# Kernel tuning notes

Hardware: AMD Instinct MI355X
Metric: run time of the kernel (lower is better)

Reference implementation:

```python
import jax, jax.numpy as jnp
import numpy as np

PZ = 16          # partition_size
ITERS = 3        # soft_skel iterations
ADP_SMOOTH = 1e-08
A = 0.5
B = 0.5
THRESHOLD = 0.8


def _blockify(x, pz):
    # x: (N, C, Z, X, Y) -> (N*nz*nx*ny, C, pz, pz, pz), loop order N,z,x,y
    N, C, Z, X, Y = x.shape
    nz, nx, ny = Z // pz, X // pz, Y // pz
    x = x.reshape(N, C, nz, pz, nx, pz, ny, pz)
    x = x.transpose(0, 2, 4, 6, 1, 3, 5, 7)
    return x.reshape(N * nz * nx * ny, C, pz, pz, pz)


def _maxpool3d(x, win, pad):
    # torch max_pool pads with -inf
    return jax.lax.reduce_window(
        x, -jnp.inf, jax.lax.max,
        (1, 1) + win, (1, 1, 1, 1, 1),
        ((0, 0), (0, 0), (pad[0], pad[0]), (pad[1], pad[1]), (pad[2], pad[2])))


def _minpool3d(x, win, pad):
    # -maxpool(-x) == minpool with +inf padding
    return jax.lax.reduce_window(
        x, jnp.inf, jax.lax.min,
        (1, 1) + win, (1, 1, 1, 1, 1),
        ((0, 0), (0, 0), (pad[0], pad[0]), (pad[1], pad[1]), (pad[2], pad[2])))


def _soft_erode(img):
    p1 = _minpool3d(img, (3, 1, 1), (1, 0, 0))
    p2 = _minpool3d(img, (1, 3, 1), (0, 1, 0))
    p3 = _minpool3d(img, (1, 1, 3), (0, 0, 1))
    return jnp.minimum(jnp.minimum(p1, p2), p3)


def _soft_dilate(img):
    return _maxpool3d(img, (3, 3, 3), (1, 1, 1))


def _soft_skel(img, iters):
    img1 = _soft_dilate(_soft_erode(img))
    skel = jax.nn.relu(img - img1)
    for _ in range(iters):
        img = _soft_erode(img)
        img1 = _soft_dilate(_soft_erode(img))
        delta = jax.nn.relu(img - img1)
        skel = skel + jax.nn.relu(delta - skel * delta)
    return skel


def _laplacian_bdr(x):
    # 3x3x3 kernel: all -1 with center 26; per-block conv, zero padding 1
    k = -jnp.ones((27,), dtype=x.dtype).at[13].set(26.0).reshape(1, 1, 3, 3, 3)
    b = jax.lax.conv_general_dilated(
        x, k, window_strides=(1, 1, 1), padding=[(1, 1)] * 3,
        dimension_numbers=('NCDHW', 'OIDHW', 'NCDHW'))
    # clamp(min=0) then threshold at 0.1 -> binary map (zero gradient, as in torch)
    return (b > 0.1).astype(x.dtype)


def _per_channel_dice(p, g, eps=1e-6):
    C = p.shape[1]
    pf = jnp.moveaxis(p, 1, 0).reshape(C, -1)
    gf = jnp.moveaxis(g, 1, 0).reshape(C, -1)
    intersect = jnp.sum(pf * gf, axis=-1)
    denom = jnp.sum(pf * pf, axis=-1) + jnp.sum(gf * gf, axis=-1)
    return 2.0 * intersect / jnp.maximum(denom, eps)


def _tversky_terms(p_blk, g_blk):
    # blocks: (M, C, pz, pz, pz) -> per-block adaptive Tversky loss sum
    M = p_blk.shape[0]
    pf = p_blk.reshape(M, -1)
    gf = g_blk.reshape(M, -1)
    tp = jnp.sum(gf * pf, axis=1)
    fn = jnp.sum(gf * (1.0 - pf), axis=1)
    fp = jnp.sum((1.0 - gf) * pf, axis=1)
    alpha = A + B * ((fp + ADP_SMOOTH) / (fp + fn + ADP_SMOOTH))
    beta = A + B * ((fn + ADP_SMOOTH) / (fp + fn + ADP_SMOOTH))
    return jnp.sum(1.0 - (tp + ADP_SMOOTH) / (tp + alpha * fp + beta * fn + ADP_SMOOTH))


def _forward(pred, groundtruth, w1, w2):
    dice_coeff = jnp.mean(_per_channel_dice(pred, groundtruth))
    dice_loss = 1.0 - jnp.mean(_per_channel_dice(pred, groundtruth))

    p_blk = _blockify(pred, PZ)          # (M, 1, pz, pz, pz)
    g_blk = _blockify(groundtruth, PZ)
    M = p_blk.shape[0]

    pre_bdr = _laplacian_bdr(p_blk)
    gt_bdr = _laplacian_bdr(g_blk)
    pre_cl = _soft_skel(p_blk, ITERS)
    gt_cl = _soft_skel(g_blk, ITERS)

    loss_bdr = _tversky_terms(pre_bdr, gt_bdr)
    loss_cl = _tversky_terms(pre_cl, gt_cl)

    w1s, w2s = w1[0], w2[0]
    edge_loss = (w1s ** -2 * loss_bdr + w2s ** -2 * loss_cl) / (2.0 * M) \
        + jnp.log(1.0 + jnp.abs(w1s) * jnp.abs(w2s))

    return jnp.where(dice_coeff < THRESHOLD, dice_loss, dice_loss + edge_loss)


def setup_inputs() -> dict:
    key = jax.random.key(0)
    k1, k2 = jax.random.split(key)
    shape = (2, 1, 192, 192, 192)
    gt = (jax.random.uniform(k1, shape, dtype=jnp.float32) > 0.7).astype(jnp.float32)
    # pred close to gt so dice_coeff > threshold and the adaptive branch runs
    pred = jnp.clip(gt * 0.9 + 0.05 + 0.02 * jax.random.normal(k2, shape, dtype=jnp.float32), 0.0, 1.0)
    return {
        'pred': pred,
        'groundtruth': gt,
        'w1': jnp.ones((1,), dtype=jnp.float32),
        'w2': jnp.ones((1,), dtype=jnp.float32),
    }


def reference(pred, groundtruth, w1, w2):
    return _forward(pred, groundtruth, w1, w2)
```

## Files before the change

kernel.cpp:

```cpp
#include <hip/hip_runtime.h>
#include <cmath>

#define NBLK 3456

template<int CTRL>
__device__ __forceinline__ int updpp(int oldv, int v) {
  return __builtin_amdgcn_update_dpp(oldv, v, CTRL, 0xF, 0xF, false);
}
__device__ __forceinline__ float nbr_lo_f(float v, float pad, bool ylo) {
  float t = __int_as_float(updpp<0x111>(__float_as_int(pad), __float_as_int(v)));
  return ylo ? pad : t;
}
__device__ __forceinline__ float nbr_hi_f(float v, float pad, bool yhi) {
  float t = __int_as_float(updpp<0x101>(__float_as_int(pad), __float_as_int(v)));
  return yhi ? pad : t;
}
__device__ __forceinline__ unsigned nbr_lo_u(unsigned v, unsigned pad, bool ylo) {
  unsigned t = (unsigned)updpp<0x111>((int)pad, (int)v);
  return ylo ? pad : t;
}
__device__ __forceinline__ unsigned nbr_hi_u(unsigned v, unsigned pad, bool yhi) {
  unsigned t = (unsigned)updpp<0x101>((int)pad, (int)v);
  return yhi ? pad : t;
}

#define COL_IDX(c, xx) (((c)*18 + (xx) + 1)*16 + y)

__global__ __launch_bounds__(256)
void fused_blocks(const float* __restrict__ pred, const float* __restrict__ gtp,
                  float* __restrict__ ws)
{
  __shared__ float4   bufE[1152];
  __shared__ float4   bufT[1152];
  __shared__ unsigned m_ex[288];
  __shared__ float    red[36];

  const int tid = threadIdx.x;
  const int x = tid >> 4;
  const int y = tid & 15;
  const bool ylo = (y == 0), yhi = (y == 15);

  const int b  = blockIdx.x;
  const int n  = b / 1728;
  const int r  = b - n * 1728;
  const int bz = r / 144;
  const int r2 = r - bz * 144;
  const int bx = r2 / 12;
  const int by = r2 - bx * 12;

  const size_t base = (size_t)(n * 192 + bz * 16) * 36864
                    + (size_t)(bx * 16 + x) * 192 + (size_t)(by * 16 + y);

  const float INF = __builtin_inff();

  if (tid < 128) {
    const int c  = tid >> 5;
    const int xi = ((tid >> 4) & 1) ? 17 : 0;
    const int yy = tid & 15;
    const int idx = (c * 18 + xi) * 16 + yy;
    bufE[idx] = make_float4(INF, INF, INF, INF);
    bufT[idx] = make_float4(0.f, 0.f, 0.f, 0.f);
  }

  float p[16];
  #pragma unroll
  for (int z = 0; z < 16; ++z) p[z] = pred[base + (size_t)z * 36864];

  float sp2 = 0.f;
  #pragma unroll
  for (int z = 0; z < 16; ++z) sp2 = fmaf(p[z], p[z], sp2);

  #pragma unroll
  for (int c = 0; c < 4; ++c)
    bufE[COL_IDX(c, x)] = make_float4(p[4*c], p[4*c+1], p[4*c+2], p[4*c+3]);

  __syncthreads();

  float szy[16];
  {
    float sy[16];
    #pragma unroll
    for (int z = 0; z < 16; ++z) {
      float v = p[z];
      sy[z] = v + nbr_lo_f(v, 0.f, ylo) + nbr_hi_f(v, 0.f, yhi);
    }
    #pragma unroll
    for (int z = 0; z < 16; ++z) {
      float s = sy[z];
      if (z > 0)  s += sy[z-1];
      if (z < 15) s += sy[z+1];
      szy[z] = s;
    }
  }
  #pragma unroll
  for (int c = 0; c < 4; ++c)
    bufT[COL_IDX(c, x)] = make_float4(szy[4*c], szy[4*c+1], szy[4*c+2], szy[4*c+3]);
  __syncthreads();

  unsigned pm_bdr = 0u;
  #pragma unroll
  for (int c = 0; c < 4; ++c) {
    float4 a4 = bufT[COL_IDX(c, x - 1)];
    float4 b4 = bufT[COL_IDX(c, x + 1)];
    float sm0 = a4.x + b4.x, sm1 = a4.y + b4.y, sm2 = a4.z + b4.z, sm3 = a4.w + b4.w;
    float bb0 = fmaf(27.f, p[4*c+0], -(szy[4*c+0] + sm0));
    float bb1 = fmaf(27.f, p[4*c+1], -(szy[4*c+1] + sm1));
    float bb2 = fmaf(27.f, p[4*c+2], -(szy[4*c+2] + sm2));
    float bb3 = fmaf(27.f, p[4*c+3], -(szy[4*c+3] + sm3));
    if (bb0 > 0.1f) pm_bdr |= (1u << (4*c+0));
    if (bb1 > 0.1f) pm_bdr |= (1u << (4*c+1));
    if (bb2 > 0.1f) pm_bdr |= (1u << (4*c+2));
    if (bb3 > 0.1f) pm_bdr |= (1u << (4*c+3));
  }
  __syncthreads();
  if (tid < 128) {
    const int c  = tid >> 5;
    const int xi = ((tid >> 4) & 1) ? 17 : 0;
    const int yy = tid & 15;
    bufT[(c * 18 + xi) * 16 + yy] = make_float4(-INF, -INF, -INF, -INF);
  }

  float cur[16], skl[16];
  #pragma unroll
  for (int z = 0; z < 16; ++z) { cur[z] = p[z]; skl[z] = 0.f; }

  for (int k = 0; k < 4; ++k) {
    float xm[16], xp[16], en[16];
    #pragma unroll
    for (int c = 0; c < 4; ++c) {
      float4 a4 = bufE[COL_IDX(c, x - 1)];
      float4 b4 = bufE[COL_IDX(c, x + 1)];
      xm[4*c] = a4.x; xm[4*c+1] = a4.y; xm[4*c+2] = a4.z; xm[4*c+3] = a4.w;
      xp[4*c] = b4.x; xp[4*c+1] = b4.y; xp[4*c+2] = b4.z; xp[4*c+3] = b4.w;
    }
    #pragma unroll
    for (int z = 0; z < 16; ++z) {
      float v = cur[z];
      float m = fminf(v, fminf(nbr_lo_f(v, INF, ylo), nbr_hi_f(v, INF, yhi)));
      if (z > 0)  m = fminf(m, cur[z-1]);
      if (z < 15) m = fminf(m, cur[z+1]);
      en[z] = fminf(m, fminf(xm[z], xp[z]));
    }
    __syncthreads();
    #pragma unroll
    for (int c = 0; c < 4; ++c)
      bufE[COL_IDX(c, x)] = make_float4(en[4*c], en[4*c+1], en[4*c+2], en[4*c+3]);
    float ty[16], tz[16];
    #pragma unroll
    for (int z = 0; z < 16; ++z) {
      float v = en[z];
      ty[z] = fmaxf(v, fmaxf(nbr_lo_f(v, -INF, ylo), nbr_hi_f(v, -INF, yhi)));
    }
    #pragma unroll
    for (int z = 0; z < 16; ++z) {
      float m = ty[z];
      if (z > 0)  m = fmaxf(m, ty[z-1]);
      if (z < 15) m = fmaxf(m, ty[z+1]);
      tz[z] = m;
    }
    __syncthreads();
    #pragma unroll
    for (int c = 0; c < 4; ++c)
      bufT[COL_IDX(c, x)] = make_float4(tz[4*c], tz[4*c+1], tz[4*c+2], tz[4*c+3]);
    __syncthreads();
    #pragma unroll
    for (int c = 0; c < 4; ++c) {
      float4 a4 = bufT[COL_IDX(c, x - 1)];
      float4 b4 = bufT[COL_IDX(c, x + 1)];
      float dm[4] = {fmaxf(a4.x, b4.x), fmaxf(a4.y, b4.y),
                     fmaxf(a4.z, b4.z), fmaxf(a4.w, b4.w)};
      #pragma unroll
      for (int j = 0; j < 4; ++j) {
        const int z = 4*c + j;
        float D = fmaxf(tz[z], dm[j]);
        float delta = fmaxf(cur[z] - D, 0.f);
        skl[z] += fmaxf(fmaf(-skl[z], delta, delta), 0.f);
        cur[z] = en[z];
      }
    }
  }

  float spg = 0.f;
  unsigned gm = 0u;
  {
    float g[16];
    #pragma unroll
    for (int z = 0; z < 16; ++z) g[z] = gtp[base + (size_t)z * 36864];
    #pragma unroll
    for (int z = 0; z < 16; ++z) {
      spg = fmaf(p[z], g[z], spg);
      if (g[z] > 0.5f) gm |= (1u << z);
    }
  }

  unsigned ly  = gm & nbr_lo_u(gm, 0u, ylo) & nbr_hi_u(gm, 0u, yhi);
  unsigned lzy = ly & (ly >> 1) & ((ly << 1) & 0xFFFFu);
  m_ex[(x + 1) * 16 + y] = lzy;
  if (tid < 32) m_ex[((tid >> 4) ? 17 : 0) * 16 + (tid & 15)] = 0u;
  __syncthreads();
  unsigned gm_bdr = gm & ~(m_ex[x * 16 + y] & lzy & m_ex[(x + 2) * 16 + y]);

  unsigned curm = gm, sklm = 0u;
  for (int k = 0; k < 4; ++k) {
    __syncthreads();
    m_ex[(x + 1) * 16 + y] = curm;
    if (tid < 32) m_ex[((tid >> 4) ? 17 : 0) * 16 + (tid & 15)] = 0xFFFFu;
    __syncthreads();
    unsigned em = curm
        & nbr_lo_u(curm, 0xFFFFu, ylo) & nbr_hi_u(curm, 0xFFFFu, yhi)
        & ((curm >> 1) | 0x8000u) & ((curm << 1) | 1u)
        & m_ex[x * 16 + y] & m_ex[(x + 2) * 16 + y];
    em &= 0xFFFFu;
    unsigned dy  = em | nbr_lo_u(em, 0u, ylo) | nbr_hi_u(em, 0u, yhi);
    unsigned dzy = (dy | (dy >> 1) | (dy << 1)) & 0xFFFFu;
    __syncthreads();
    m_ex[(x + 1) * 16 + y] = dzy;
    if (tid < 32) m_ex[((tid >> 4) ? 17 : 0) * 16 + (tid & 15)] = 0u;
    __syncthreads();
    unsigned D = m_ex[x * 16 + y] | dzy | m_ex[(x + 2) * 16 + y];
    sklm |= curm & ~D;
    curm = em;
  }

  float vals[9];
  {
    float tcl = 0.f, scl = 0.f;
    #pragma unroll
    for (int z = 0; z < 16; ++z) {
      scl += skl[z];
      tcl += ((sklm >> z) & 1u) ? skl[z] : 0.f;
    }
    vals[0] = tcl;
    vals[1] = scl;
    vals[2] = (float)__popc(sklm);
    vals[3] = (float)__popc(pm_bdr & gm_bdr);
    vals[4] = (float)__popc(pm_bdr);
    vals[5] = (float)__popc(gm_bdr);
    vals[6] = spg;
    vals[7] = sp2;
    vals[8] = (float)__popc(gm);
  }
  #pragma unroll
  for (int j = 0; j < 9; ++j) {
    float v = vals[j];
    #pragma unroll
    for (int off = 32; off; off >>= 1) v += __shfl_xor(v, off);
    vals[j] = v;
  }
  if ((tid & 63) == 0) {
    #pragma unroll
    for (int j = 0; j < 9; ++j) red[(tid >> 6) * 9 + j] = vals[j];
  }
  __syncthreads();
  if (tid == 0) {
    float t[9];
    #pragma unroll
    for (int j = 0; j < 9; ++j) t[j] = red[j] + red[9 + j] + red[18 + j] + red[27 + j];
    const float s = 1e-8f;
    float tp = t[3], fp = t[4] - t[3], fn = t[5] - t[3];
    float den = fp + fn + s;
    float alpha = 0.5f + 0.5f * ((fp + s) / den);
    float beta  = 0.5f + 0.5f * ((fn + s) / den);
    float lb = 1.f - (tp + s) / (tp + alpha * fp + beta * fn + s);
    float tpc = t[0], fpc = t[1] - t[0], fnc = t[2] - t[0];
    float denc = fpc + fnc + s;
    float alphac = 0.5f + 0.5f * ((fpc + s) / denc);
    float betac  = 0.5f + 0.5f * ((fnc + s) / denc);
    float lc = 1.f - (tpc + s) / (tpc + alphac * fpc + betac * fnc + s);
    float* o = ws + (size_t)b * 8;
    o[0] = lb; o[1] = lc; o[2] = t[6]; o[3] = t[7]; o[4] = t[8];
  }
}

__global__ __launch_bounds__(256)
void finalize_kernel(const float* __restrict__ ws, const float* __restrict__ w1p,
                     const float* __restrict__ w2p, float* __restrict__ out)
{
  __shared__ double red2[20];
  double a[5] = {0.0, 0.0, 0.0, 0.0, 0.0};
  for (int i = threadIdx.x; i < NBLK; i += 256) {
    const float* o = ws + (size_t)i * 8;
    a[0] += (double)o[0];
    a[1] += (double)o[1];
    a[2] += (double)o[2];
    a[3] += (double)o[3];
    a[4] += (double)o[4];
  }
  #pragma unroll
  for (int j = 0; j < 5; ++j) {
    double v = a[j];
    #pragma unroll
    for (int off = 32; off; off >>= 1) v += __shfl_xor(v, off);
    if ((threadIdx.x & 63) == 0) red2[(threadIdx.x >> 6) * 5 + j] = v;
  }
  __syncthreads();
  if (threadIdx.x == 0) {
    double t[5];
    #pragma unroll
    for (int j = 0; j < 5; ++j) t[j] = red2[j] + red2[5 + j] + red2[10 + j] + red2[15 + j];
    double denom = t[3] + t[4];
    if (denom < 1e-6) denom = 1e-6;
    double dice = 2.0 * t[2] / denom;
    double dl = 1.0 - dice;
    double w1 = (double)w1p[0], w2 = (double)w2p[0];
    double edge = (t[0] / (w1 * w1) + t[1] / (w2 * w2)) / (2.0 * (double)NBLK)
                + log(1.0 + fabs(w1) * fabs(w2));
    out[0] = (float)((dice < 0.8) ? dl : (dl + edge));
  }
}

extern "C" void kernel_launch(void* const* d_in, const int* in_sizes, int n_in,
                              void* d_out, int out_size, void* d_ws, size_t ws_size,
                              hipStream_t stream)
{
  const float* pred = (const float*)d_in[0];
  const float* gtp  = (const float*)d_in[1];
  const float* w1   = (const float*)d_in[2];
  const float* w2   = (const float*)d_in[3];
  float* ws = (float*)d_ws;

  fused_blocks<<<NBLK, 256, 0, stream>>>(pred, gtp, ws);
  finalize_kernel<<<1, 256, 0, stream>>>(ws, w1, w2, (float*)d_out);
}
```

Measured before the change: 178.3 us.

## Merge LDS buffers, use DPP bound_ctrl padding, fuse finalize via atomics

Collapses the two float4 shared buffers and mask and reduction arrays into one aliased LDS buffer, and sets launch bounds to 8 blocks per CU to raise occupancy. Replaces the explicit y-boundary selects with DPP bound_ctrl zero-fill or keep-self semantics, which is valid for min/max since the lane itself is already in the window. Moves the ground-truth load up to overlap with the pred load. Drops the separate finalize kernel in favour of float atomics plus a last-block ticket, with a memset to zero the accumulators. Float atomic accumulation order is nondeterministic, and the lower per-thread register budget from the occupancy target may cause spills.

```diff
diff --git a/kernel.cpp b/kernel.cpp
--- a/kernel.cpp
+++ b/kernel.cpp
@@ -3,42 +3,43 @@
 
 #define NBLK 3456
 
+#define DPP_SHR1 0x111
+#define DPP_SHL1 0x101
+
 template<int CTRL>
-__device__ __forceinline__ int updpp(int oldv, int v) {
-  return __builtin_amdgcn_update_dpp(oldv, v, CTRL, 0xF, 0xF, false);
-}
-__device__ __forceinline__ float nbr_lo_f(float v, float pad, bool ylo) {
-  float t = __int_as_float(updpp<0x111>(__float_as_int(pad), __float_as_int(v)));
-  return ylo ? pad : t;
-}
-__device__ __forceinline__ float nbr_hi_f(float v, float pad, bool yhi) {
-  float t = __int_as_float(updpp<0x101>(__float_as_int(pad), __float_as_int(v)));
-  return yhi ? pad : t;
-}
-__device__ __forceinline__ unsigned nbr_lo_u(unsigned v, unsigned pad, bool ylo) {
-  unsigned t = (unsigned)updpp<0x111>((int)pad, (int)v);
-  return ylo ? pad : t;
-}
-__device__ __forceinline__ unsigned nbr_hi_u(unsigned v, unsigned pad, bool yhi) {
-  unsigned t = (unsigned)updpp<0x101>((int)pad, (int)v);
-  return yhi ? pad : t;
+__device__ __forceinline__ float dpp_keep_f(float v) {
+  return __int_as_float(__builtin_amdgcn_update_dpp(
+      __float_as_int(v), __float_as_int(v), CTRL, 0xF, 0xF, false));
+}
+template<int CTRL>
+__device__ __forceinline__ float dpp_zero_f(float v) {
+  return __int_as_float(__builtin_amdgcn_update_dpp(
+      0, __float_as_int(v), CTRL, 0xF, 0xF, true));
+}
+template<int CTRL>
+__device__ __forceinline__ unsigned dpp_keep_u(unsigned v) {
+  return (unsigned)__builtin_amdgcn_update_dpp((int)v, (int)v, CTRL, 0xF, 0xF, false);
+}
+template<int CTRL>
+__device__ __forceinline__ unsigned dpp_zero_u(unsigned v) {
+  return (unsigned)__builtin_amdgcn_update_dpp(0, (int)v, CTRL, 0xF, 0xF, true);
 }
 
 #define COL_IDX(c, xx) (((c)*18 + (xx) + 1)*16 + y)
 
-__global__ __launch_bounds__(256)
+__global__ __launch_bounds__(256, 8)
 void fused_blocks(const float* __restrict__ pred, const float* __restrict__ gtp,
-                  float* __restrict__ ws)
+                  const float* __restrict__ w1p, const float* __restrict__ w2p,
+                  float* __restrict__ acc,
+                  float* __restrict__ out)
 {
-  __shared__ float4   bufE[1152];
-  __shared__ float4   bufT[1152];
-  __shared__ unsigned m_ex[288];
-  __shared__ float    red[36];
+  __shared__ float4 buf[1152];
+  unsigned* m_ex = (unsigned*)buf;
+  float*    red  = ((float*)buf) + 512;
 
   const int tid = threadIdx.x;
   const int x = tid >> 4;
   const int y = tid & 15;
-  const bool ylo = (y == 0), yhi = (y == 15);
 
   const int b  = blockIdx.x;
   const int n  = b / 1728;
@@ -53,28 +54,28 @@
 
   const float INF = __builtin_inff();
 
-  if (tid < 128) {
-    const int c  = tid >> 5;
-    const int xi = ((tid >> 4) & 1) ? 17 : 0;
-    const int yy = tid & 15;
-    const int idx = (c * 18 + xi) * 16 + yy;
-    bufE[idx] = make_float4(INF, INF, INF, INF);
-    bufT[idx] = make_float4(0.f, 0.f, 0.f, 0.f);
-  }
+  auto write_pads = [&](float pv) {
+    if (tid < 128) {
+      const int c  = tid >> 5;
+      const int xi = ((tid >> 4) & 1) ? 17 : 0;
+      const int yy = tid & 15;
+      buf[(c * 18 + xi) * 16 + yy] = make_float4(pv, pv, pv, pv);
+    }
+  };
 
   float p[16];
   #pragma unroll
   for (int z = 0; z < 16; ++z) p[z] = pred[base + (size_t)z * 36864];
 
-  float sp2 = 0.f;
-  #pragma unroll
-  for (int z = 0; z < 16; ++z) sp2 = fmaf(p[z], p[z], sp2);
-
-  #pragma unroll
-  for (int c = 0; c < 4; ++c)
-    bufE[COL_IDX(c, x)] = make_float4(p[4*c], p[4*c+1], p[4*c+2], p[4*c+3]);
-
-  __syncthreads();
+  unsigned gm = 0u;
+  float sp2 = 0.f, spg = 0.f;
+  #pragma unroll
+  for (int z = 0; z < 16; ++z) {
+    float gz = gtp[base + (size_t)z * 36864];
+    sp2 = fmaf(p[z], p[z], sp2);
+    spg = fmaf(p[z], gz, spg);
+    if (gz > 0.5f) gm |= (1u << z);
+  }
 
   float szy[16];
   {
@@ -82,7 +83,7 @@
     #pragma unroll
     for (int z = 0; z < 16; ++z) {
       float v = p[z];
-      sy[z] = v + nbr_lo_f(v, 0.f, ylo) + nbr_hi_f(v, 0.f, yhi);
+      sy[z] = v + dpp_zero_f<DPP_SHR1>(v) + dpp_zero_f<DPP_SHL1>(v);
     }
     #pragma unroll
     for (int z = 0; z < 16; ++z) {
@@ -94,62 +95,58 @@
   }
   #pragma unroll
   for (int c = 0; c < 4; ++c)
-    bufT[COL_IDX(c, x)] = make_float4(szy[4*c], szy[4*c+1], szy[4*c+2], szy[4*c+3]);
+    buf[COL_IDX(c, x)] = make_float4(szy[4*c], szy[4*c+1], szy[4*c+2], szy[4*c+3]);
+  write_pads(0.f);
   __syncthreads();
 
   unsigned pm_bdr = 0u;
   #pragma unroll
   for (int c = 0; c < 4; ++c) {
-    float4 a4 = bufT[COL_IDX(c, x - 1)];
-    float4 b4 = bufT[COL_IDX(c, x + 1)];
-    float sm0 = a4.x + b4.x, sm1 = a4.y + b4.y, sm2 = a4.z + b4.z, sm3 = a4.w + b4.w;
-    float bb0 = fmaf(27.f, p[4*c+0], -(szy[4*c+0] + sm0));
-    float bb1 = fmaf(27.f, p[4*c+1], -(szy[4*c+1] + sm1));
-    float bb2 = fmaf(27.f, p[4*c+2], -(szy[4*c+2] + sm2));
-    float bb3 = fmaf(27.f, p[4*c+3], -(szy[4*c+3] + sm3));
-    if (bb0 > 0.1f) pm_bdr |= (1u << (4*c+0));
-    if (bb1 > 0.1f) pm_bdr |= (1u << (4*c+1));
-    if (bb2 > 0.1f) pm_bdr |= (1u << (4*c+2));
-    if (bb3 > 0.1f) pm_bdr |= (1u << (4*c+3));
-  }
-  __syncthreads();
-  if (tid < 128) {
-    const int c  = tid >> 5;
-    const int xi = ((tid >> 4) & 1) ? 17 : 0;
-    const int yy = tid & 15;
-    bufT[(c * 18 + xi) * 16 + yy] = make_float4(-INF, -INF, -INF, -INF);
-  }
+    float4 a4 = buf[COL_IDX(c, x - 1)];
+    float4 b4 = buf[COL_IDX(c, x + 1)];
+    float sm[4] = {a4.x + b4.x, a4.y + b4.y, a4.z + b4.z, a4.w + b4.w};
+    #pragma unroll
+    for (int j = 0; j < 4; ++j) {
+      const int z = 4*c + j;
+      float bb = fmaf(27.f, p[z], -(szy[z] + sm[j]));
+      if (bb > 0.1f) pm_bdr |= (1u << z);
+    }
+  }
+  __syncthreads();
+
+  #pragma unroll
+  for (int c = 0; c < 4; ++c)
+    buf[COL_IDX(c, x)] = make_float4(p[4*c], p[4*c+1], p[4*c+2], p[4*c+3]);
+  write_pads(INF);
+  __syncthreads();
 
   float cur[16], skl[16];
   #pragma unroll
   for (int z = 0; z < 16; ++z) { cur[z] = p[z]; skl[z] = 0.f; }
 
   for (int k = 0; k < 4; ++k) {
-    float xm[16], xp[16], en[16];
+    float xm[16], xp[16];
     #pragma unroll
     for (int c = 0; c < 4; ++c) {
-      float4 a4 = bufE[COL_IDX(c, x - 1)];
-      float4 b4 = bufE[COL_IDX(c, x + 1)];
+      float4 a4 = buf[COL_IDX(c, x - 1)];
+      float4 b4 = buf[COL_IDX(c, x + 1)];
       xm[4*c] = a4.x; xm[4*c+1] = a4.y; xm[4*c+2] = a4.z; xm[4*c+3] = a4.w;
       xp[4*c] = b4.x; xp[4*c+1] = b4.y; xp[4*c+2] = b4.z; xp[4*c+3] = b4.w;
     }
+    float en[16];
     #pragma unroll
     for (int z = 0; z < 16; ++z) {
       float v = cur[z];
-      float m = fminf(v, fminf(nbr_lo_f(v, INF, ylo), nbr_hi_f(v, INF, yhi)));
+      float m = fminf(v, fminf(dpp_keep_f<DPP_SHR1>(v), dpp_keep_f<DPP_SHL1>(v)));
       if (z > 0)  m = fminf(m, cur[z-1]);
       if (z < 15) m = fminf(m, cur[z+1]);
       en[z] = fminf(m, fminf(xm[z], xp[z]));
     }
-    __syncthreads();
-    #pragma unroll
-    for (int c = 0; c < 4; ++c)
-      bufE[COL_IDX(c, x)] = make_float4(en[4*c], en[4*c+1], en[4*c+2], en[4*c+3]);
     float ty[16], tz[16];
     #pragma unroll
     for (int z = 0; z < 16; ++z) {
       float v = en[z];
-      ty[z] = fmaxf(v, fmaxf(nbr_lo_f(v, -INF, ylo), nbr_hi_f(v, -INF, yhi)));
+      ty[z] = fmaxf(v, fmaxf(dpp_keep_f<DPP_SHR1>(v), dpp_keep_f<DPP_SHL1>(v)));
     }
     #pragma unroll
     for (int z = 0; z < 16; ++z) {
@@ -161,12 +158,13 @@
     __syncthreads();
     #pragma unroll
     for (int c = 0; c < 4; ++c)
-      bufT[COL_IDX(c, x)] = make_float4(tz[4*c], tz[4*c+1], tz[4*c+2], tz[4*c+3]);
+      buf[COL_IDX(c, x)] = make_float4(tz[4*c], tz[4*c+1], tz[4*c+2], tz[4*c+3]);
+    write_pads(-INF);
     __syncthreads();
     #pragma unroll
     for (int c = 0; c < 4; ++c) {
-      float4 a4 = bufT[COL_IDX(c, x - 1)];
-      float4 b4 = bufT[COL_IDX(c, x + 1)];
+      float4 a4 = buf[COL_IDX(c, x - 1)];
+      float4 b4 = buf[COL_IDX(c, x + 1)];
       float dm[4] = {fmaxf(a4.x, b4.x), fmaxf(a4.y, b4.y),
                      fmaxf(a4.z, b4.z), fmaxf(a4.w, b4.w)};
       #pragma unroll
@@ -178,22 +176,18 @@
         cur[z] = en[z];
       }
     }
-  }
-
-  float spg = 0.f;
-  unsigned gm = 0u;
-  {
-    float g[16];
-    #pragma unroll
-    for (int z = 0; z < 16; ++z) g[z] = gtp[base + (size_t)z * 36864];
-    #pragma unroll
-    for (int z = 0; z < 16; ++z) {
-      spg = fmaf(p[z], g[z], spg);
-      if (g[z] > 0.5f) gm |= (1u << z);
-    }
-  }
-
-  unsigned ly  = gm & nbr_lo_u(gm, 0u, ylo) & nbr_hi_u(gm, 0u, yhi);
+    if (k < 3) {
+      __syncthreads();
+      #pragma unroll
+      for (int c = 0; c < 4; ++c)
+        buf[COL_IDX(c, x)] = make_float4(en[4*c], en[4*c+1], en[4*c+2], en[4*c+3]);
+      write_pads(INF);
+      __syncthreads();
+    }
+  }
+  __syncthreads();
+
+  unsigned ly  = gm & dpp_zero_u<DPP_SHR1>(gm) & dpp_zero_u<DPP_SHL1>(gm);
   unsigned lzy = ly & (ly >> 1) & ((ly << 1) & 0xFFFFu);
   m_ex[(x + 1) * 16 + y] = lzy;
   if (tid < 32) m_ex[((tid >> 4) ? 17 : 0) * 16 + (tid & 15)] = 0u;
@@ -207,11 +201,11 @@
     if (tid < 32) m_ex[((tid >> 4) ? 17 : 0) * 16 + (tid & 15)] = 0xFFFFu;
     __syncthreads();
     unsigned em = curm
-        & nbr_lo_u(curm, 0xFFFFu, ylo) & nbr_hi_u(curm, 0xFFFFu, yhi)
+        & dpp_keep_u<DPP_SHR1>(curm) & dpp_keep_u<DPP_SHL1>(curm)
         & ((curm >> 1) | 0x8000u) & ((curm << 1) | 1u)
         & m_ex[x * 16 + y] & m_ex[(x + 2) * 16 + y];
     em &= 0xFFFFu;
-    unsigned dy  = em | nbr_lo_u(em, 0u, ylo) | nbr_hi_u(em, 0u, yhi);
+    unsigned dy  = em | dpp_keep_u<DPP_SHR1>(em) | dpp_keep_u<DPP_SHL1>(em);
     unsigned dzy = (dy | (dy >> 1) | (dy << 1)) & 0xFFFFu;
     __syncthreads();
     m_ex[(x + 1) * 16 + y] = dzy;
@@ -267,45 +261,30 @@
     float alphac = 0.5f + 0.5f * ((fpc + s) / denc);
     float betac  = 0.5f + 0.5f * ((fnc + s) / denc);
     float lc = 1.f - (tpc + s) / (tpc + alphac * fpc + betac * fnc + s);
-    float* o = ws + (size_t)b * 8;
-    o[0] = lb; o[1] = lc; o[2] = t[6]; o[3] = t[7]; o[4] = t[8];
-  }
-}
-
-__global__ __launch_bounds__(256)
-void finalize_kernel(const float* __restrict__ ws, const float* __restrict__ w1p,
-                     const float* __restrict__ w2p, float* __restrict__ out)
-{
-  __shared__ double red2[20];
-  double a[5] = {0.0, 0.0, 0.0, 0.0, 0.0};
-  for (int i = threadIdx.x; i < NBLK; i += 256) {
-    const float* o = ws + (size_t)i * 8;
-    a[0] += (double)o[0];
-    a[1] += (double)o[1];
-    a[2] += (double)o[2];
-    a[3] += (double)o[3];
-    a[4] += (double)o[4];
-  }
-  #pragma unroll
-  for (int j = 0; j < 5; ++j) {
-    double v = a[j];
-    #pragma unroll
-    for (int off = 32; off; off >>= 1) v += __shfl_xor(v, off);
-    if ((threadIdx.x & 63) == 0) red2[(threadIdx.x >> 6) * 5 + j] = v;
-  }
-  __syncthreads();
-  if (threadIdx.x == 0) {
-    double t[5];
-    #pragma unroll
-    for (int j = 0; j < 5; ++j) t[j] = red2[j] + red2[5 + j] + red2[10 + j] + red2[15 + j];
-    double denom = t[3] + t[4];
-    if (denom < 1e-6) denom = 1e-6;
-    double dice = 2.0 * t[2] / denom;
-    double dl = 1.0 - dice;
-    double w1 = (double)w1p[0], w2 = (double)w2p[0];
-    double edge = (t[0] / (w1 * w1) + t[1] / (w2 * w2)) / (2.0 * (double)NBLK)
-                + log(1.0 + fabs(w1) * fabs(w2));
-    out[0] = (float)((dice < 0.8) ? dl : (dl + edge));
+
+    atomicAdd(&acc[0], lb);
+    atomicAdd(&acc[1], lc);
+    atomicAdd(&acc[2], t[6]);
+    atomicAdd(&acc[3], t[7]);
+    atomicAdd(&acc[4], t[8]);
+    __threadfence();
+    unsigned* cnt = (unsigned*)(acc + 5);
+    unsigned ticket = atomicAdd(cnt, 1u);
+    if (ticket == NBLK - 1) {
+      double t0 = (double)atomicAdd(&acc[0], 0.f);
+      double t1 = (double)atomicAdd(&acc[1], 0.f);
+      double t2 = (double)atomicAdd(&acc[2], 0.f);
+      double t3 = (double)atomicAdd(&acc[3], 0.f);
+      double t4 = (double)atomicAdd(&acc[4], 0.f);
+      double denom = t3 + t4;
+      if (denom < 1e-6) denom = 1e-6;
+      double dice = 2.0 * t2 / denom;
+      double dl = 1.0 - dice;
+      double w1 = (double)w1p[0], w2 = (double)w2p[0];
+      double edge = (t0 / (w1 * w1) + t1 / (w2 * w2)) / (2.0 * (double)NBLK)
+                  + log(1.0 + fabs(w1) * fabs(w2));
+      out[0] = (float)((dice < 0.8) ? dl : (dl + edge));
+    }
   }
 }
 
@@ -317,8 +296,8 @@
   const float* gtp  = (const float*)d_in[1];
   const float* w1   = (const float*)d_in[2];
   const float* w2   = (const float*)d_in[3];
-  float* ws = (float*)d_ws;
-
-  fused_blocks<<<NBLK, 256, 0, stream>>>(pred, gtp, ws);
-  finalize_kernel<<<1, 256, 0, stream>>>(ws, w1, w2, (float*)d_out);
-}
+
+  hipMemsetAsync(d_ws, 0, 32, stream);
+  fused_blocks<<<NBLK, 256, 0, stream>>>(pred, gtp, w1, w2,
+                                         (float*)d_ws, (float*)d_out);
+}
```

Measured after the change: 665.6 us. +273.4%, slower.
